# Kernel tuning notes

Hardware: AMD Instinct MI355X
Metric: run time of the kernel (lower is better)

## Reference

```python
import jax, jax.numpy as jnp
import numpy as np

D = 256      # d_model
H = 8        # n_heads
L = 4        # n_levels
P = 4        # n_points
DFF = 1024   # d_ffn
DH = D // H  # head dim
SPATIAL = np.array([[100, 100], [50, 50], [25, 25], [13, 13]], dtype=np.int64)  # (H_l, W_l)
LV = int((SPATIAL[:, 0] * SPATIAL[:, 1]).sum())  # 13294 flattened memory tokens


def layer_norm(x, w, b, eps=1e-5):
    m = jnp.mean(x, -1, keepdims=True)
    v = jnp.mean((x - m) ** 2, -1, keepdims=True)
    return (x - m) * jax.lax.rsqrt(v + eps) * w + b


def setup_inputs() -> dict:
    key = jax.random.key(0)
    ks = jax.random.split(key, 16)
    nq, bs = 900, 8

    def w(k, shape, s=0.02):
        return jax.random.normal(k, shape, dtype=jnp.float32) * s

    return {
        "tgt": jax.random.normal(ks[0], (nq, bs, D), jnp.float32),
        "tgt_query_pos": jax.random.normal(ks[1], (nq, bs, D), jnp.float32),
        "tgt_reference_points": jax.random.uniform(ks[2], (nq, bs, L, 2), jnp.float32),
        "memory": jax.random.normal(ks[3], (LV, bs, D), jnp.float32),
        "sa_Wqkv": w(ks[4], (3 * D, D)), "sa_bqkv": jnp.zeros((3 * D,), jnp.float32),
        "sa_Wo": w(ks[5], (D, D)), "sa_bo": jnp.zeros((D,), jnp.float32),
        "ln1_w": jnp.ones((D,), jnp.float32), "ln1_b": jnp.zeros((D,), jnp.float32),
        "ln2_w": jnp.ones((D,), jnp.float32), "ln2_b": jnp.zeros((D,), jnp.float32),
        "ln3_w": jnp.ones((D,), jnp.float32), "ln3_b": jnp.zeros((D,), jnp.float32),
        "ca_Woff": w(ks[6], (H * L * P * 2, D)), "ca_boff": w(ks[7], (H * L * P * 2,), 0.5),
        "ca_Wattn": w(ks[8], (H * L * P, D)), "ca_battn": jnp.zeros((H * L * P,), jnp.float32),
        "ca_Wval": w(ks[9], (D, D)), "ca_bval": jnp.zeros((D,), jnp.float32),
        "ca_Wout": w(ks[10], (D, D)), "ca_bout": jnp.zeros((D,), jnp.float32),
        "ffn_W1": w(ks[11], (DFF, D)), "ffn_b1": jnp.zeros((DFF,), jnp.float32),
        "ffn_W2": w(ks[12], (D, DFF)), "ffn_b2": jnp.zeros((D,), jnp.float32),
        "memory_key_padding_mask": jnp.zeros((bs, LV), jnp.bool_),
        "memory_spatial_shapes": jnp.asarray(SPATIAL),
    }


def msdeform_attn(query, ref, value, mask, shapes_np,
                  Woff, boff, Wattn, battn, Wval, bval, Wout, bout):
    # query: [bs,nq,D], ref: [bs,nq,L,2], value: [bs,lv,D], mask: [bs,lv]
    bs, nq, _ = query.shape
    lv = value.shape[1]
    v = value @ Wval.T + bval
    v = jnp.where(mask[:, :, None], 0.0, v)
    v = v.reshape(bs, lv, H, DH).transpose(0, 2, 1, 3)  # [bs,H,lv,DH]
    off = (query @ Woff.T + boff).reshape(bs, nq, H, L, P, 2)
    aw = jax.nn.softmax((query @ Wattn.T + battn).reshape(bs, nq, H, L * P), -1)
    aw = aw.reshape(bs, nq, H, L, P)
    # offset normalizer is [W_l, H_l]
    norm = jnp.asarray(shapes_np[:, ::-1].copy(), jnp.float32)  # [L,2]
    loc = ref[:, :, None, :, None, :] + off / norm[None, None, None, :, None, :]
    out = jnp.zeros((bs, nq, H, DH), jnp.float32)
    start = 0
    for l in range(L):
        Hl, Wl = int(shapes_np[l, 0]), int(shapes_np[l, 1])
        vf = v[:, :, start:start + Hl * Wl]  # [bs,H,Hl*Wl,DH]
        start += Hl * Wl
        # grid_sample(align_corners=False) pixel coords
        x = loc[:, :, :, l, :, 0] * Wl - 0.5  # [bs,nq,H,P]
        y = loc[:, :, :, l, :, 1] * Hl - 0.5
        x0 = jnp.floor(x); y0 = jnp.floor(y)
        fx = x - x0; fy = y - y0
        x0i = x0.astype(jnp.int32); y0i = y0.astype(jnp.int32)

        def gather(yi, xi):
            valid = ((xi >= 0) & (xi < Wl) & (yi >= 0) & (yi < Hl)).astype(jnp.float32)
            idx = jnp.clip(yi, 0, Hl - 1) * Wl + jnp.clip(xi, 0, Wl - 1)
            idx_t = idx.transpose(0, 2, 1, 3).reshape(bs, H, nq * P, 1)
            g = jnp.take_along_axis(vf, idx_t, axis=2)  # [bs,H,nq*P,DH]
            return g * valid.transpose(0, 2, 1, 3).reshape(bs, H, nq * P, 1)

        def wgt(w):
            return w.transpose(0, 2, 1, 3).reshape(bs, H, nq * P, 1)

        samp = (gather(y0i, x0i) * wgt((1 - fx) * (1 - fy))
                + gather(y0i, x0i + 1) * wgt(fx * (1 - fy))
                + gather(y0i + 1, x0i) * wgt((1 - fx) * fy)
                + gather(y0i + 1, x0i + 1) * wgt(fx * fy))
        samp = samp.reshape(bs, H, nq, P, DH)
        out = out + jnp.einsum('bhqpd,bqhp->bqhd', samp, aw[:, :, :, l])
    return out.reshape(bs, nq, D) @ Wout.T + bout


def reference(tgt, tgt_query_pos, tgt_reference_points, memory,
              sa_Wqkv, sa_bqkv, sa_Wo, sa_bo,
              ln1_w, ln1_b, ln2_w, ln2_b, ln3_w, ln3_b,
              ca_Woff, ca_boff, ca_Wattn, ca_battn, ca_Wval, ca_bval, ca_Wout, ca_bout,
              ffn_W1, ffn_b1, ffn_W2, ffn_b2,
              memory_key_padding_mask, memory_spatial_shapes):
    shapes_np = np.asarray(memory_spatial_shapes)  # static per trace
    nq, bs, _ = tgt.shape
    # --- self attention (post-LN, residual) ---
    q = tgt + tgt_query_pos
    qp = (q @ sa_Wqkv[:D].T + sa_bqkv[:D]).reshape(nq, bs, H, DH)
    kp = (q @ sa_Wqkv[D:2 * D].T + sa_bqkv[D:2 * D]).reshape(nq, bs, H, DH)
    vp = (tgt @ sa_Wqkv[2 * D:].T + sa_bqkv[2 * D:]).reshape(nq, bs, H, DH)
    scores = jnp.einsum('qbhd,kbhd->bhqk', qp, kp) * (1.0 / float(np.sqrt(DH)))
    attn = jax.nn.softmax(scores, -1)
    o = jnp.einsum('bhqk,kbhd->qbhd', attn, vp).reshape(nq, bs, D) @ sa_Wo.T + sa_bo
    tgt = layer_norm(tgt + o, ln2_w, ln2_b)
    # --- multi-scale deformable cross attention ---
    query = (tgt + tgt_query_pos).transpose(1, 0, 2)      # [bs,nq,D]
    ref = tgt_reference_points.transpose(1, 0, 2, 3)      # [bs,nq,L,2]
    val = memory.transpose(1, 0, 2)                       # [bs,lv,D]
    ca = msdeform_attn(query, ref, val, memory_key_padding_mask, shapes_np,
                       ca_Woff, ca_boff, ca_Wattn, ca_battn,
                       ca_Wval, ca_bval, ca_Wout, ca_bout).transpose(1, 0, 2)
    tgt = layer_norm(tgt + ca, ln1_w, ln1_b)
    # --- FFN ---
    t2 = jax.nn.relu(tgt @ ffn_W1.T + ffn_b1) @ ffn_W2.T + ffn_b2
    return layer_norm(tgt + t2, ln3_w, ln3_b)
```

## Files before the change

### kernel.cpp

```cpp
#include <hip/hip_runtime.h>
#include <hip/hip_bf16.h>

#define NQ   900
#define BSZ  8
#define DM   256
#define NH   8
#define DHD  32
#define DFF_ 1024
#define LVTOT 13294
#define NTOK (NQ*BSZ)
#define MVAL (LVTOT*BSZ)

typedef __attribute__((ext_vector_type(8))) short bf16x8;
typedef __attribute__((ext_vector_type(4))) short bf16x4;
typedef __attribute__((ext_vector_type(4))) float f32x4;
typedef unsigned int u32;

__device__ __forceinline__ unsigned short f2bf(float x) {
  union { __hip_bfloat16 h; unsigned short u; } cv;
  cv.h = __float2bfloat16(x);
  return cv.u;
}
__device__ __forceinline__ float bf2f(unsigned short u) {
  union { __hip_bfloat16 h; unsigned short u; } cv;
  cv.u = u;
  return __bfloat162float(cv.h);
}

__device__ __forceinline__ void gl_lds16(const void* gsrc, void* ldst) {
  __builtin_amdgcn_global_load_lds(
      (const __attribute__((address_space(1))) u32*)gsrc,
      (__attribute__((address_space(3))) u32*)ldst, 16, 0, 0);
}

__global__ __launch_bounds__(256) void prep_kernel(
    const float* p0, const float* p1, const float* p2, const float* p3,
    const float* p4, const float* p5, const float* p6, const float* p7,
    unsigned short* wdst,
    const float* a, const float* b, unsigned short* qdst,
    const float* boff, const float* battn, float* bcat) {
  int bid = blockIdx.x, tid = threadIdx.x;
  if (bid < 496) {
    long i8 = ((long)bid * 256 + tid) * 8;
    const float* src; long off;
    if      (i8 < 196608) { src = p0; off = i8; }
    else if (i8 < 262144) { src = p1; off = i8 - 196608; }
    else if (i8 < 327680) { src = p2; off = i8 - 262144; }
    else if (i8 < 393216) { src = p3; off = i8 - 327680; }
    else if (i8 < 425984) { src = p4; off = i8 - 393216; }
    else if (i8 < 491520) { src = p5; off = i8 - 425984; }
    else if (i8 < 753664) { src = p6; off = i8 - 491520; }
    else                  { src = p7; off = i8 - 753664; }
    float4 x = *(const float4*)(src + off);
    float4 y = *(const float4*)(src + off + 4);
    bf16x8 v;
    v[0] = (short)f2bf(x.x); v[1] = (short)f2bf(x.y);
    v[2] = (short)f2bf(x.z); v[3] = (short)f2bf(x.w);
    v[4] = (short)f2bf(y.x); v[5] = (short)f2bf(y.y);
    v[6] = (short)f2bf(y.z); v[7] = (short)f2bf(y.w);
    *(bf16x8*)(wdst + i8) = v;
  } else if (bid < 496 + 900) {
    int i = (bid - 496) * 256 + tid;
    float4 a0 = ((const float4*)a)[i * 2], a1 = ((const float4*)a)[i * 2 + 1];
    float4 b0 = ((const float4*)b)[i * 2], b1 = ((const float4*)b)[i * 2 + 1];
    bf16x8 v;
    v[0] = (short)f2bf(a0.x + b0.x); v[1] = (short)f2bf(a0.y + b0.y);
    v[2] = (short)f2bf(a0.z + b0.z); v[3] = (short)f2bf(a0.w + b0.w);
    v[4] = (short)f2bf(a1.x + b1.x); v[5] = (short)f2bf(a1.y + b1.y);
    v[6] = (short)f2bf(a1.z + b1.z); v[7] = (short)f2bf(a1.w + b1.w);
    *(bf16x8*)(qdst + (long)i * 8) = v;
  } else {
    int i = (bid - 1396) * 256 + tid;
    if (i < 256) bcat[i] = boff[i];
    else if (i < 384) bcat[i] = battn[i - 256];
  }
}


struct B3 {
  const void* A[3];
  const unsigned short* W[3];
  const float* bias[3];
  void* C[3];
  int M[3], ldc[3], af32[3], blk0[3], nx[3];
};

__global__ __launch_bounds__(256, 4) void gemm_batch3_kernel(B3 ops) {
  constexpr int K = 256, NSTEP = 4;
  __shared__ alignas(16) unsigned char As[32768];
  __shared__ alignas(16) unsigned char Bs[16384];
  int bid = blockIdx.x;
  int oi = (bid >= ops.blk0[2]) ? 2 : (bid >= ops.blk0[1] ? 1 : 0);
  int rel = bid - ops.blk0[oi];
  int nx = ops.nx[oi];
  int bx = rel % nx, by = rel / nx;
  const void* Araw = ops.A[oi];
  const unsigned short* W = ops.W[oi];
  const float* bias = ops.bias[oi];
  void* C = ops.C[oi];
  int M = ops.M[oi], ldc = ops.ldc[oi], AF32 = ops.af32[oi];

  int tid = threadIdx.x;
  int l = tid & 63, w = tid >> 6;
  int lr = l & 15, lg = l >> 4;
  int wr = w >> 1, wc = w & 1;
  int n0 = bx * 128, m0 = by * 128;
  int phase = by & (NSTEP - 1);

  f32x4 acc[4][4];
#pragma unroll
  for (int m = 0; m < 4; m++)
#pragma unroll
    for (int n = 0; n < 4; n++) acc[m][n] = (f32x4){0.f, 0.f, 0.f, 0.f};

  for (int tt = 0; tt < NSTEP; tt++) {
    int t = tt + phase; if (t >= NSTEP) t -= NSTEP;
    int k0 = t * 64;
    __syncthreads();
#pragma unroll
    for (int i4 = 0; i4 < 4; i4++) {
      int i = i4 * 4 + w;
      int row = i * 8 + (l >> 3);
      int sc = (l & 7) ^ (row & 7);
      gl_lds16(W + (long)(n0 + row) * K + k0 + sc * 8, Bs + i * 1024 + l * 16);
    }
    if (AF32) {
      const float* Af = (const float*)Araw;
#pragma unroll
      for (int i4 = 0; i4 < 8; i4++) {
        int i = i4 * 4 + w;
        int row = i * 4 + (l >> 4);
        int g = m0 + row; if (g >= M) g = M - 1;
        int sc = (l & 15) ^ (row & 15);
        gl_lds16(Af + (long)g * K + k0 + sc * 4, As + i * 1024 + l * 16);
      }
    } else {
      const unsigned short* A = (const unsigned short*)Araw;
#pragma unroll
      for (int i4 = 0; i4 < 4; i4++) {
        int i = i4 * 4 + w;
        int row = i * 8 + (l >> 3);
        int g = m0 + row; if (g >= M) g = M - 1;
        int sc = (l & 7) ^ (row & 7);
        gl_lds16(A + (long)g * K + k0 + sc * 8, As + i * 1024 + l * 16);
      }
    }
    __syncthreads();
#pragma unroll
    for (int sk = 0; sk < 2; sk++) {
      bf16x8 af[4], bfr[4];
      if (AF32) {
#pragma unroll
        for (int m = 0; m < 4; m++) {
          int row = wr * 64 + m * 16 + lr;
          int ca = (sk * 8 + lg * 2) ^ (row & 15);
          int cb = (sk * 8 + lg * 2 + 1) ^ (row & 15);
          f32x4 fa = *(const f32x4*)(As + row * 256 + ca * 16);
          f32x4 fb = *(const f32x4*)(As + row * 256 + cb * 16);
          bf16x8 v;
          v[0] = (short)f2bf(fa[0]); v[1] = (short)f2bf(fa[1]);
          v[2] = (short)f2bf(fa[2]); v[3] = (short)f2bf(fa[3]);
          v[4] = (short)f2bf(fb[0]); v[5] = (short)f2bf(fb[1]);
          v[6] = (short)f2bf(fb[2]); v[7] = (short)f2bf(fb[3]);
          af[m] = v;
        }
      } else {
#pragma unroll
        for (int m = 0; m < 4; m++) {
          int row = wr * 64 + m * 16 + lr;
          int c = (sk * 4 + lg) ^ (row & 7);
          af[m] = *(const bf16x8*)(As + row * 128 + c * 16);
        }
      }
#pragma unroll
      for (int n = 0; n < 4; n++) {
        int row = wc * 64 + n * 16 + lr;
        int c = (sk * 4 + lg) ^ (row & 7);
        bfr[n] = *(const bf16x8*)(Bs + row * 128 + c * 16);
      }
#pragma unroll
      for (int m = 0; m < 4; m++)
#pragma unroll
        for (int n = 0; n < 4; n++)
          acc[m][n] = __builtin_amdgcn_mfma_f32_16x16x32_bf16(af[m], bfr[n], acc[m][n], 0, 0, 0);
    }
  }

  float bv[4];
#pragma unroll
  for (int ni = 0; ni < 4; ni++) bv[ni] = bias[n0 + wc * 64 + ni * 16 + lr];
#pragma unroll
  for (int mi = 0; mi < 4; mi++) {
#pragma unroll
    for (int r = 0; r < 4; r++) {
      int row = m0 + wr * 64 + mi * 16 + lg * 4 + r;
      if (row < M) {
#pragma unroll
        for (int ni = 0; ni < 4; ni++) {
          int col = n0 + wc * 64 + ni * 16 + lr;
          ((unsigned short*)C)[(long)row * ldc + col] = f2bf(acc[mi][ni][r] + bv[ni]);
        }
      }
    }
  }
}

template <int AF32, int OUT_BF16, int RELU, int NSTEP>
__global__ __launch_bounds__(256, 4) void gemm_s_kernel(
    const void* __restrict__ Araw, const unsigned short* __restrict__ W,
    const float* __restrict__ bias, void* __restrict__ C,
    int M, int ldc) {
  constexpr int K = NSTEP * 64;
  constexpr int ABYTES = AF32 ? 32768 : 16384;
  __shared__ alignas(16) unsigned char As[ABYTES];
  __shared__ alignas(16) unsigned char Bs[16384];
  int tid = threadIdx.x;
  int l = tid & 63, w = tid >> 6;
  int lr = l & 15, lg = l >> 4;
  int wr = w >> 1, wc = w & 1;
  int n0 = blockIdx.x * 128, m0 = blockIdx.y * 128;
  int phase = blockIdx.y & (NSTEP - 1);

  f32x4 acc[4][4];
#pragma unroll
  for (int m = 0; m < 4; m++)
#pragma unroll
    for (int n = 0; n < 4; n++) acc[m][n] = (f32x4){0.f, 0.f, 0.f, 0.f};

  for (int tt = 0; tt < NSTEP; tt++) {
    int t = tt + phase; if (t >= NSTEP) t -= NSTEP;
    int k0 = t * 64;
    __syncthreads();
#pragma unroll
    for (int i4 = 0; i4 < 4; i4++) {
      int i = i4 * 4 + w;
      int row = i * 8 + (l >> 3);
      int sc = (l & 7) ^ (row & 7);
      gl_lds16(W + (long)(n0 + row) * K + k0 + sc * 8, Bs + i * 1024 + l * 16);
    }
    if (AF32) {
      const float* Af = (const float*)Araw;
#pragma unroll
      for (int i4 = 0; i4 < 8; i4++) {
        int i = i4 * 4 + w;
        int row = i * 4 + (l >> 4);
        int g = m0 + row; if (g >= M) g = M - 1;
        int sc = (l & 15) ^ (row & 15);
        gl_lds16(Af + (long)g * K + k0 + sc * 4, As + i * 1024 + l * 16);
      }
    } else {
      const unsigned short* A = (const unsigned short*)Araw;
#pragma unroll
      for (int i4 = 0; i4 < 4; i4++) {
        int i = i4 * 4 + w;
        int row = i * 8 + (l >> 3);
        int g = m0 + row; if (g >= M) g = M - 1;
        int sc = (l & 7) ^ (row & 7);
        gl_lds16(A + (long)g * K + k0 + sc * 8, As + i * 1024 + l * 16);
      }
    }
    __syncthreads();
#pragma unroll
    for (int sk = 0; sk < 2; sk++) {
      bf16x8 af[4], bfr[4];
      if (AF32) {
#pragma unroll
        for (int m = 0; m < 4; m++) {
          int row = wr * 64 + m * 16 + lr;
          int ca = (sk * 8 + lg * 2) ^ (row & 15);
          int cb = (sk * 8 + lg * 2 + 1) ^ (row & 15);
          f32x4 fa = *(const f32x4*)(As + row * 256 + ca * 16);
          f32x4 fb = *(const f32x4*)(As + row * 256 + cb * 16);
          bf16x8 v;
          v[0] = (short)f2bf(fa[0]); v[1] = (short)f2bf(fa[1]);
          v[2] = (short)f2bf(fa[2]); v[3] = (short)f2bf(fa[3]);
          v[4] = (short)f2bf(fb[0]); v[5] = (short)f2bf(fb[1]);
          v[6] = (short)f2bf(fb[2]); v[7] = (short)f2bf(fb[3]);
          af[m] = v;
        }
      } else {
#pragma unroll
        for (int m = 0; m < 4; m++) {
          int row = wr * 64 + m * 16 + lr;
          int c = (sk * 4 + lg) ^ (row & 7);
          af[m] = *(const bf16x8*)(As + row * 128 + c * 16);
        }
      }
#pragma unroll
      for (int n = 0; n < 4; n++) {
        int row = wc * 64 + n * 16 + lr;
        int c = (sk * 4 + lg) ^ (row & 7);
        bfr[n] = *(const bf16x8*)(Bs + row * 128 + c * 16);
      }
#pragma unroll
      for (int m = 0; m < 4; m++)
#pragma unroll
        for (int n = 0; n < 4; n++)
          acc[m][n] = __builtin_amdgcn_mfma_f32_16x16x32_bf16(af[m], bfr[n], acc[m][n], 0, 0, 0);
    }
  }

  float bv[4];
#pragma unroll
  for (int ni = 0; ni < 4; ni++) bv[ni] = bias[n0 + wc * 64 + ni * 16 + lr];
#pragma unroll
  for (int mi = 0; mi < 4; mi++) {
#pragma unroll
    for (int r = 0; r < 4; r++) {
      int row = m0 + wr * 64 + mi * 16 + lg * 4 + r;
      if (row < M) {
#pragma unroll
        for (int ni = 0; ni < 4; ni++) {
          int col = n0 + wc * 64 + ni * 16 + lr;
          float v = acc[mi][ni][r] + bv[ni];
          if (RELU) v = fmaxf(v, 0.f);
          if (OUT_BF16) ((unsigned short*)C)[(long)row * ldc + col] = f2bf(v);
          else          ((float*)C)[(long)row * ldc + col] = v;
        }
      }
    }
  }
}

__global__ __launch_bounds__(256) void attn_mfma_kernel(const unsigned short* __restrict__ qkv,
                                                        unsigned short* __restrict__ out) {
  __shared__ unsigned short Vt[32][72];
  __shared__ unsigned short Ps[4][16][72];
  int tid = threadIdx.x;
  int l = tid & 63, w = tid >> 6;
  int lr = l & 15, lg = l >> 4;
  int q0 = blockIdx.x * 64;
  int h = blockIdx.y & 7, b = blockIdx.y >> 3;
  const float scale = 0.17677669529663687f;

  int qrow = q0 + w * 16 + lr;
  int qclamp = qrow < 899 ? qrow : 899;
  bf16x8 qf = *(const bf16x8*)(qkv + ((long)qclamp * 8 + b) * 768 + h * 32 + lg * 8);

  f32x4 o_acc[2];
  o_acc[0] = (f32x4){0.f, 0.f, 0.f, 0.f};
  o_acc[1] = (f32x4){0.f, 0.f, 0.f, 0.f};
  float m_run[4] = {-1e30f, -1e30f, -1e30f, -1e30f};
  float l_run[4] = {0.f, 0.f, 0.f, 0.f};

  for (int k0 = 0; k0 < NQ; k0 += 64) {
    __syncthreads();
    {
      int key = tid >> 2, dg = tid & 3;
      int kk = k0 + key; if (kk > 899) kk = 899;
      bf16x8 vv = *(const bf16x8*)(qkv + ((long)kk * 8 + b) * 768 + 512 + h * 32 + dg * 8);
#pragma unroll
      for (int j = 0; j < 8; j++) Vt[dg * 8 + j][key] = (unsigned short)vv[j];
    }
    f32x4 sg[4];
#pragma unroll
    for (int ng = 0; ng < 4; ng++) {
      int key = k0 + ng * 16 + lr; int kc = key < 899 ? key : 899;
      bf16x8 kf = *(const bf16x8*)(qkv + ((long)kc * 8 + b) * 768 + 256 + h * 32 + lg * 8);
      sg[ng] = __builtin_amdgcn_mfma_f32_16x16x32_bf16(qf, kf, (f32x4){0.f, 0.f, 0.f, 0.f}, 0, 0, 0);
    }
    float sv[4][4];
#pragma unroll
    for (int ng = 0; ng < 4; ng++) {
      bool bad = (k0 + ng * 16 + lr) >= NQ;
#pragma unroll
      for (int r = 0; r < 4; r++) sv[ng][r] = bad ? -1e30f : sg[ng][r] * scale;
    }
    float p[4][4];
#pragma unroll
    for (int r = 0; r < 4; r++) {
      float rmax = fmaxf(fmaxf(sv[0][r], sv[1][r]), fmaxf(sv[2][r], sv[3][r]));
#pragma unroll
      for (int mk = 8; mk; mk >>= 1) rmax = fmaxf(rmax, __shfl_xor(rmax, mk));
      float mnew = fmaxf(m_run[r], rmax);
      float fs = __expf(m_run[r] - mnew);
      m_run[r] = mnew;
      float ps = 0.f;
#pragma unroll
      for (int ng = 0; ng < 4; ng++) { p[ng][r] = __expf(sv[ng][r] - mnew); ps += p[ng][r]; }
#pragma unroll
      for (int mk = 8; mk; mk >>= 1) ps += __shfl_xor(ps, mk);
      l_run[r] = l_run[r] * fs + ps;
      o_acc[0][r] *= fs;
      o_acc[1][r] *= fs;
    }
#pragma unroll
    for (int ng = 0; ng < 4; ng++)
#pragma unroll
      for (int r = 0; r < 4; r++)
        Ps[w][lg * 4 + r][lr + ng * 16] = f2bf(p[ng][r]);
    __syncthreads();
#pragma unroll
    for (int ks = 0; ks < 2; ks++) {
      bf16x8 pf = *(const bf16x8*)&Ps[w][lr][ks * 32 + lg * 8];
#pragma unroll
      for (int ni = 0; ni < 2; ni++) {
        bf16x8 vf = *(const bf16x8*)&Vt[ni * 16 + lr][ks * 32 + lg * 8];
        o_acc[ni] = __builtin_amdgcn_mfma_f32_16x16x32_bf16(pf, vf, o_acc[ni], 0, 0, 0);
      }
    }
  }
#pragma unroll
  for (int r = 0; r < 4; r++) {
    int orow = q0 + w * 16 + lg * 4 + r;
    if (orow < NQ) {
      float inv = 1.f / l_run[r];
      unsigned short* op = out + ((long)orow * 8 + b) * 256 + h * 32 + lr;
      op[0]  = f2bf(o_acc[0][r] * inv);
      op[16] = f2bf(o_acc[1][r] * inv);
    }
  }
}

__device__ __forceinline__ void fetch8_acc(const unsigned short* __restrict__ vtmp, int lo, int W,
                                           int yi, int xi, int b, int col0, float wgt,
                                           float* a) {
  if ((xi < 0) | (xi >= W) | (yi < 0) | (yi >= W)) return;
  const unsigned short* p = vtmp + ((long)((lo + yi * W + xi) * BSZ + b)) * 256 + col0;
  bf16x8 r = *(const bf16x8*)p;
#pragma unroll
  for (int j = 0; j < 8; j++) a[j] += wgt * bf2f((unsigned short)r[j]);
}

__global__ __launch_bounds__(256) void sampler_kernel(const unsigned short* __restrict__ vtmp,
                                                      const float* __restrict__ oa,
                                                      const float* __restrict__ ref,
                                                      unsigned short* __restrict__ samp) {
  __shared__ float s_off[8][256];
  __shared__ float s_aw[8][128];
  __shared__ float s_ref[8][8];
  int tid = threadIdx.x;
  int t0 = blockIdx.x * 8;
#pragma unroll
  for (int k = 0; k < 8; k++) s_off[k][tid] = oa[(long)(t0 + k) * 384 + tid];
#pragma unroll
  for (int i = 0; i < 4; i++) {
    int idx = i * 256 + tid;
    int k = idx >> 7, c = idx & 127;
    s_aw[k][c] = oa[(long)(t0 + k) * 384 + 256 + c];
  }
  if (tid < 64) s_ref[tid >> 3][tid & 7] = ref[(long)(t0 + (tid >> 3)) * 8 + (tid & 7)];
  __syncthreads();
  if (tid < 64) {
    int k = tid >> 3, hh = tid & 7;
    float* p = &s_aw[k][hh * 16];
    float m = -1e30f;
#pragma unroll
    for (int j = 0; j < 16; j++) m = fmaxf(m, p[j]);
    float s = 0.f;
#pragma unroll
    for (int j = 0; j < 16; j++) { p[j] = __expf(p[j] - m); s += p[j]; }
    float inv = 1.f / s;
#pragma unroll
    for (int j = 0; j < 16; j++) p[j] *= inv;
  }
  __syncthreads();
  int w = tid >> 5;
  int l = tid & 31;
  int t = t0 + w;
  int h = l >> 2, col0 = h * 32 + (l & 3) * 8;
  int b = t & 7;
  const int Wls[4]  = {100, 50, 25, 13};
  const int lofs[4] = {0, 10000, 12500, 13125};
  float a[8];
#pragma unroll
  for (int j = 0; j < 8; j++) a[j] = 0.f;
#pragma unroll
  for (int lvl = 0; lvl < 4; lvl++) {
    int W = Wls[lvl];
    float Wf = (float)W;
    int lo = lofs[lvl];
    float rx = s_ref[w][lvl * 2 + 0], ry = s_ref[w][lvl * 2 + 1];
#pragma unroll
    for (int p = 0; p < 4; p++) {
      float ox = s_off[w][((h * 4 + lvl) * 4 + p) * 2 + 0];
      float oy = s_off[w][((h * 4 + lvl) * 4 + p) * 2 + 1];
      float x = rx * Wf + ox - 0.5f;
      float y = ry * Wf + oy - 0.5f;
      float x0f = floorf(x), y0f = floorf(y);
      float fx = x - x0f, fy = y - y0f;
      int x0 = (int)x0f, y0 = (int)y0f;
      float aa = s_aw[w][h * 16 + lvl * 4 + p];
      float w00 = aa * (1.f - fx) * (1.f - fy);
      float w01 = aa * fx * (1.f - fy);
      float w10 = aa * (1.f - fx) * fy;
      float w11 = aa * fx * fy;
      fetch8_acc(vtmp, lo, W, y0,     x0,     b, col0, w00, a);
      fetch8_acc(vtmp, lo, W, y0,     x0 + 1, b, col0, w01, a);
      fetch8_acc(vtmp, lo, W, y0 + 1, x0,     b, col0, w10, a);
      fetch8_acc(vtmp, lo, W, y0 + 1, x0 + 1, b, col0, w11, a);
    }
  }
  bf16x8 o;
#pragma unroll
  for (int j = 0; j < 8; j++) o[j] = (short)f2bf(a[j]);
  *(bf16x8*)(samp + (long)t * 256 + col0) = o;
}

__global__ __launch_bounds__(256) void ln_kernel(const float* __restrict__ x,
                                                 const float* __restrict__ res,
                                                 const float* __restrict__ w,
                                                 const float* __restrict__ bvec,
                                                 float* __restrict__ out,
                                                 unsigned short* __restrict__ out_bf,
                                                 const float* __restrict__ pos,
                                                 unsigned short* __restrict__ pos_bf,
                                                 int rows) {
  int wv = threadIdx.x >> 6, lane = threadIdx.x & 63;
  int row = blockIdx.x * 4 + wv;
  if (row >= rows) return;
  float4 xv = *(const float4*)(x + (long)row * 256 + lane * 4);
  float4 rv = *(const float4*)(res + (long)row * 256 + lane * 4);
  float v0 = xv.x + rv.x, v1 = xv.y + rv.y, v2 = xv.z + rv.z, v3 = xv.w + rv.w;
  float s = v0 + v1 + v2 + v3;
#pragma unroll
  for (int o = 32; o; o >>= 1) s += __shfl_xor(s, o);
  float mean = s * (1.f / 256.f);
  float d0 = v0 - mean, d1 = v1 - mean, d2 = v2 - mean, d3 = v3 - mean;
  float q = d0 * d0 + d1 * d1 + d2 * d2 + d3 * d3;
#pragma unroll
  for (int o = 32; o; o >>= 1) q += __shfl_xor(q, o);
  float rstd = rsqrtf(q * (1.f / 256.f) + 1e-5f);
  float4 wv4 = *(const float4*)(w + lane * 4);
  float4 bv4 = *(const float4*)(bvec + lane * 4);
  float o0 = d0 * rstd * wv4.x + bv4.x;
  float o1 = d1 * rstd * wv4.y + bv4.y;
  float o2 = d2 * rstd * wv4.z + bv4.z;
  float o3 = d3 * rstd * wv4.w + bv4.w;
  *(float4*)(out + (long)row * 256 + lane * 4) = make_float4(o0, o1, o2, o3);
  if (out_bf) {
    unsigned short* p = out_bf + (long)row * 256 + lane * 4;
    p[0] = f2bf(o0); p[1] = f2bf(o1); p[2] = f2bf(o2); p[3] = f2bf(o3);
  }
  if (pos_bf) {
    float4 pv = *(const float4*)(pos + (long)row * 256 + lane * 4);
    unsigned short* p = pos_bf + (long)row * 256 + lane * 4;
    p[0] = f2bf(o0 + pv.x); p[1] = f2bf(o1 + pv.y);
    p[2] = f2bf(o2 + pv.z); p[3] = f2bf(o3 + pv.w);
  }
}

extern "C" void kernel_launch(void* const* d_in, const int* in_sizes, int n_in,
                              void* d_out, int out_size, void* d_ws, size_t ws_size,
                              hipStream_t stream) {
  const float* tgt     = (const float*)d_in[0];
  const float* pos     = (const float*)d_in[1];
  const float* refpts  = (const float*)d_in[2];
  const float* memory  = (const float*)d_in[3];
  const float* sa_Wqkv = (const float*)d_in[4];
  const float* sa_bqkv = (const float*)d_in[5];
  const float* sa_Wo   = (const float*)d_in[6];
  const float* sa_bo   = (const float*)d_in[7];
  const float* ln1_w   = (const float*)d_in[8];
  const float* ln1_b   = (const float*)d_in[9];
  const float* ln2_w   = (const float*)d_in[10];
  const float* ln2_b   = (const float*)d_in[11];
  const float* ln3_w   = (const float*)d_in[12];
  const float* ln3_b   = (const float*)d_in[13];
  const float* ca_Woff = (const float*)d_in[14];
  const float* ca_boff = (const float*)d_in[15];
  const float* ca_Wattn= (const float*)d_in[16];
  const float* ca_battn= (const float*)d_in[17];
  const float* ca_Wval = (const float*)d_in[18];
  const float* ca_bval = (const float*)d_in[19];
  const float* ca_Wout = (const float*)d_in[20];
  const float* ca_bout = (const float*)d_in[21];
  const float* ffn_W1  = (const float*)d_in[22];
  const float* ffn_b1  = (const float*)d_in[23];
  const float* ffn_W2  = (const float*)d_in[24];
  const float* ffn_b2  = (const float*)d_in[25];

  char* ws = (char*)d_ws;
  float*          buf_ca = (float*)(ws);
  float*          buf_t3 = (float*)(ws + 8388608);
  unsigned short* t3_bf  = (unsigned short*)(ws + 16777216);
  unsigned short* buf_h  = (unsigned short*)(ws + 20971520);
  float*          buf_f  = (float*)(ws + 36700160);
  float*          bias_cat = (float*)(ws + 44072960);
  unsigned short* buf_v  = (unsigned short*)(ws + 54452224);
  unsigned short* wts    = (unsigned short*)(ws + 112590848);
  unsigned short* buf_q  = (unsigned short*)(ws + 114622464);
  unsigned short* buf_qkv= (unsigned short*)(ws + 118308864);
  float*          buf_oa = (float*)(ws + 118308864);
  unsigned short* buf_o  = (unsigned short*)(ws + 129368064);
  unsigned short* buf_smp= (unsigned short*)(ws + 129368064);
  float*          buf_t2 = (float*)(ws + 133054464);

  const unsigned short* w_qkv = wts + 0;
  const unsigned short* w_o   = wts + 196608;
  const unsigned short* w_val = wts + 262144;
  const unsigned short* w_oa  = wts + 327680;
  const unsigned short* w_out = wts + 425984;
  const unsigned short* w_f1  = wts + 491520;
  const unsigned short* w_f2  = wts + 753664;

  dim3 blk(256);

  prep_kernel<<<1398, blk, 0, stream>>>(sa_Wqkv, sa_Wo, ca_Wval, ca_Woff, ca_Wattn,
                                        ca_Wout, ffn_W1, ffn_W2, wts,
                                        tgt, pos, buf_q, ca_boff, ca_battn, bias_cat);

  B3 ops;
  ops.A[0] = memory;   ops.W[0] = w_val;           ops.bias[0] = ca_bval;      ops.C[0] = buf_v;
  ops.M[0] = MVAL;     ops.ldc[0] = 256;           ops.af32[0] = 1;            ops.nx[0] = 2;
  ops.A[1] = buf_q;    ops.W[1] = w_qkv;           ops.bias[1] = sa_bqkv;      ops.C[1] = buf_qkv;
  ops.M[1] = NTOK;     ops.ldc[1] = 768;           ops.af32[1] = 0;            ops.nx[1] = 4;
  ops.A[2] = tgt;      ops.W[2] = w_qkv + 512*256; ops.bias[2] = sa_bqkv + 512; ops.C[2] = buf_qkv + 512;
  ops.M[2] = NTOK;     ops.ldc[2] = 768;           ops.af32[2] = 1;            ops.nx[2] = 2;
  ops.blk0[0] = 0; ops.blk0[1] = 1662; ops.blk0[2] = 1890;
  gemm_batch3_kernel<<<2004, blk, 0, stream>>>(ops);

  attn_mfma_kernel<<<dim3(15, 64), blk, 0, stream>>>(buf_qkv, buf_o);
  gemm_s_kernel<0, 0, 0, 4><<<dim3(2, 57), blk, 0, stream>>>(buf_o, w_o, sa_bo,
                                                             buf_t2, NTOK, 256);
  ln_kernel<<<1800, blk, 0, stream>>>(buf_t2, tgt, ln2_w, ln2_b, buf_t2, nullptr,
                                      pos, buf_q, NTOK);
  gemm_s_kernel<0, 0, 0, 4><<<dim3(3, 57), blk, 0, stream>>>(buf_q, w_oa, bias_cat,
                                                             buf_oa, NTOK, 384);
  sampler_kernel<<<NTOK / 8, blk, 0, stream>>>(buf_v, buf_oa, refpts, buf_smp);
  gemm_s_kernel<0, 0, 0, 4><<<dim3(2, 57), blk, 0, stream>>>(buf_smp, w_out, ca_bout,
                                                             buf_ca, NTOK, 256);
  ln_kernel<<<1800, blk, 0, stream>>>(buf_ca, buf_t2, ln1_w, ln1_b, buf_t3, t3_bf,
                                      nullptr, nullptr, NTOK);
  gemm_s_kernel<0, 1, 1, 4><<<dim3(8, 57), blk, 0, stream>>>(t3_bf, w_f1, ffn_b1,
                                                             buf_h, NTOK, 1024);
  gemm_s_kernel<0, 0, 0, 16><<<dim3(2, 57), blk, 0, stream>>>(buf_h, w_f2, ffn_b2,
                                                              buf_f, NTOK, 256);
  ln_kernel<<<1800, blk, 0, stream>>>(buf_f, buf_t3, ln3_w, ln3_b, (float*)d_out, nullptr,
                                      nullptr, nullptr, NTOK);
}
```

Before: 217.8 us.

## Fuse output-projection GEMMs with residual add and LayerNorm

Adds a gemm_ln kernel in which each block computes a full 64x256 row tile, adds bias and residual, reduces row mean and variance across warps through shared memory, and writes the normalized output plus an optional bf16 copy (with or without the positional embedding added). This replaces three GEMM+ln_kernel pairs, removing the separate LayerNorm launches and the fp32 intermediate round trips through memory. The cost is a grid of only 113 blocks and a one-pass variance formula that is less numerically robust.

```diff
diff --git a/kernel.cpp b/kernel.cpp
--- a/kernel.cpp
+++ b/kernel.cpp
@@ -76,7 +76,6 @@
   }
 }
 
-
 struct B3 {
   const void* A[3];
   const unsigned short* W[3];
@@ -320,6 +319,126 @@
       }
     }
   }
+}
+
+template <int NSTEP, int OUT2>
+__global__ __launch_bounds__(256, 4) void gemm_ln_kernel(
+    const unsigned short* __restrict__ A, const unsigned short* __restrict__ W,
+    const float* __restrict__ bias, const float* __restrict__ res,
+    const float* __restrict__ lnw, const float* __restrict__ lnb,
+    float* __restrict__ out, unsigned short* __restrict__ out2,
+    const float* __restrict__ pos, int M) {
+  constexpr int K = NSTEP * 64;
+  __shared__ alignas(16) unsigned char As[8192];
+  __shared__ alignas(16) unsigned char Bs[32768];
+  __shared__ float psum[4][64], psq[4][64];
+  int tid = threadIdx.x;
+  int l = tid & 63, w = tid >> 6;
+  int lr = l & 15, lg = l >> 4;
+  int m0 = blockIdx.x * 64;
+  int phase = blockIdx.x & (NSTEP - 1);
+
+  f32x4 acc[4][4];
+#pragma unroll
+  for (int m = 0; m < 4; m++)
+#pragma unroll
+    for (int n = 0; n < 4; n++) acc[m][n] = (f32x4){0.f, 0.f, 0.f, 0.f};
+
+  for (int tt = 0; tt < NSTEP; tt++) {
+    int t = tt + phase; if (t >= NSTEP) t -= NSTEP;
+    int k0 = t * 64;
+    __syncthreads();
+#pragma unroll
+    for (int j = 0; j < 2; j++) {
+      int lin = j * 256 + tid;
+      int row = lin >> 3, s = lin & 7;
+      int g = m0 + row; if (g >= M) g = M - 1;
+      int sc = s ^ (row & 7);
+      gl_lds16(A + (long)g * K + k0 + sc * 8, As + lin * 16);
+    }
+#pragma unroll
+    for (int j = 0; j < 8; j++) {
+      int lin = j * 256 + tid;
+      int row = lin >> 3, s = lin & 7;
+      int sc = s ^ (row & 7);
+      gl_lds16(W + (long)row * K + k0 + sc * 8, Bs + lin * 16);
+    }
+    __syncthreads();
+#pragma unroll
+    for (int sk = 0; sk < 2; sk++) {
+      bf16x8 af[4], bfr[4];
+#pragma unroll
+      for (int m = 0; m < 4; m++) {
+        int row = m * 16 + lr;
+        int c = (sk * 4 + lg) ^ (row & 7);
+        af[m] = *(const bf16x8*)(As + row * 128 + c * 16);
+      }
+#pragma unroll
+      for (int n = 0; n < 4; n++) {
+        int row = w * 64 + n * 16 + lr;
+        int c = (sk * 4 + lg) ^ (row & 7);
+        bfr[n] = *(const bf16x8*)(Bs + row * 128 + c * 16);
+      }
+#pragma unroll
+      for (int m = 0; m < 4; m++)
+#pragma unroll
+        for (int n = 0; n < 4; n++)
+          acc[m][n] = __builtin_amdgcn_mfma_f32_16x16x32_bf16(af[m], bfr[n], acc[m][n], 0, 0, 0);
+    }
+  }
+
+  float bv[4], lw[4], lb[4];
+#pragma unroll
+  for (int ni = 0; ni < 4; ni++) {
+    int col = w * 64 + ni * 16 + lr;
+    bv[ni] = bias[col]; lw[ni] = lnw[col]; lb[ni] = lnb[col];
+  }
+#pragma unroll
+  for (int mi = 0; mi < 4; mi++)
+#pragma unroll
+    for (int r2 = 0; r2 < 4; r2++) {
+      int row = m0 + mi * 16 + lg * 4 + r2;
+      int rc = row < M ? row : M - 1;
+#pragma unroll
+      for (int ni = 0; ni < 4; ni++)
+        acc[mi][ni][r2] += bv[ni] + res[(long)rc * 256 + w * 64 + ni * 16 + lr];
+    }
+#pragma unroll
+  for (int mi = 0; mi < 4; mi++)
+#pragma unroll
+    for (int r2 = 0; r2 < 4; r2++) {
+      float s = acc[mi][0][r2] + acc[mi][1][r2] + acc[mi][2][r2] + acc[mi][3][r2];
+      float q = acc[mi][0][r2] * acc[mi][0][r2] + acc[mi][1][r2] * acc[mi][1][r2] +
+                acc[mi][2][r2] * acc[mi][2][r2] + acc[mi][3][r2] * acc[mi][3][r2];
+#pragma unroll
+      for (int o = 1; o < 16; o <<= 1) { s += __shfl_xor(s, o); q += __shfl_xor(q, o); }
+      if (lr == 0) {
+        int lrow = mi * 16 + lg * 4 + r2;
+        psum[w][lrow] = s; psq[w][lrow] = q;
+      }
+    }
+  __syncthreads();
+#pragma unroll
+  for (int mi = 0; mi < 4; mi++)
+#pragma unroll
+    for (int r2 = 0; r2 < 4; r2++) {
+      int lrow = mi * 16 + lg * 4 + r2;
+      int row = m0 + lrow;
+      if (row >= M) continue;
+      float tot = psum[0][lrow] + psum[1][lrow] + psum[2][lrow] + psum[3][lrow];
+      float tq  = psq[0][lrow] + psq[1][lrow] + psq[2][lrow] + psq[3][lrow];
+      float mean = tot * (1.f / 256.f);
+      float var = tq * (1.f / 256.f) - mean * mean;
+      float rstd = rsqrtf(var + 1e-5f);
+#pragma unroll
+      for (int ni = 0; ni < 4; ni++) {
+        int col = w * 64 + ni * 16 + lr;
+        float o = (acc[mi][ni][r2] - mean) * rstd * lw[ni] + lb[ni];
+        out[(long)row * 256 + col] = o;
+        if (OUT2 == 1) out2[(long)row * 256 + col] = f2bf(o);
+        if (OUT2 == 2) out2[(long)row * 256 + col] = f2bf(o + pos[(long)row * 256 + col]);
+      }
+    }
 }
 
 __global__ __launch_bounds__(256) void attn_mfma_kernel(const unsigned short* __restrict__ qkv,
@@ -495,49 +614,6 @@
 #pragma unroll
   for (int j = 0; j < 8; j++) o[j] = (short)f2bf(a[j]);
   *(bf16x8*)(samp + (long)t * 256 + col0) = o;
-}
-
-__global__ __launch_bounds__(256) void ln_kernel(const float* __restrict__ x,
-                                                 const float* __restrict__ res,
-                                                 const float* __restrict__ w,
-                                                 const float* __restrict__ bvec,
-                                                 float* __restrict__ out,
-                                                 unsigned short* __restrict__ out_bf,
-                                                 const float* __restrict__ pos,
-                                                 unsigned short* __restrict__ pos_bf,
-                                                 int rows) {
-  int wv = threadIdx.x >> 6, lane = threadIdx.x & 63;
-  int row = blockIdx.x * 4 + wv;
-  if (row >= rows) return;
-  float4 xv = *(const float4*)(x + (long)row * 256 + lane * 4);
-  float4 rv = *(const float4*)(res + (long)row * 256 + lane * 4);
-  float v0 = xv.x + rv.x, v1 = xv.y + rv.y, v2 = xv.z + rv.z, v3 = xv.w + rv.w;
-  float s = v0 + v1 + v2 + v3;
-#pragma unroll
-  for (int o = 32; o; o >>= 1) s += __shfl_xor(s, o);
-  float mean = s * (1.f / 256.f);
-  float d0 = v0 - mean, d1 = v1 - mean, d2 = v2 - mean, d3 = v3 - mean;
-  float q = d0 * d0 + d1 * d1 + d2 * d2 + d3 * d3;
-#pragma unroll
-  for (int o = 32; o; o >>= 1) q += __shfl_xor(q, o);
-  float rstd = rsqrtf(q * (1.f / 256.f) + 1e-5f);
-  float4 wv4 = *(const float4*)(w + lane * 4);
-  float4 bv4 = *(const float4*)(bvec + lane * 4);
-  float o0 = d0 * rstd * wv4.x + bv4.x;
-  float o1 = d1 * rstd * wv4.y + bv4.y;
-  float o2 = d2 * rstd * wv4.z + bv4.z;
-  float o3 = d3 * rstd * wv4.w + bv4.w;
-  *(float4*)(out + (long)row * 256 + lane * 4) = make_float4(o0, o1, o2, o3);
-  if (out_bf) {
-    unsigned short* p = out_bf + (long)row * 256 + lane * 4;
-    p[0] = f2bf(o0); p[1] = f2bf(o1); p[2] = f2bf(o2); p[3] = f2bf(o3);
-  }
-  if (pos_bf) {
-    float4 pv = *(const float4*)(pos + (long)row * 256 + lane * 4);
-    unsigned short* p = pos_bf + (long)row * 256 + lane * 4;
-    p[0] = f2bf(o0 + pv.x); p[1] = f2bf(o1 + pv.y);
-    p[2] = f2bf(o2 + pv.z); p[3] = f2bf(o3 + pv.w);
-  }
 }
 
 extern "C" void kernel_launch(void* const* d_in, const int* in_sizes, int n_in,
@@ -575,7 +651,6 @@
   float*          buf_t3 = (float*)(ws + 8388608);
   unsigned short* t3_bf  = (unsigned short*)(ws + 16777216);
   unsigned short* buf_h  = (unsigned short*)(ws + 20971520);
-  float*          buf_f  = (float*)(ws + 36700160);
   float*          bias_cat = (float*)(ws + 44072960);
   unsigned short* buf_v  = (unsigned short*)(ws + 54452224);
   unsigned short* wts    = (unsigned short*)(ws + 112590848);
@@ -611,21 +686,17 @@
   gemm_batch3_kernel<<<2004, blk, 0, stream>>>(ops);
 
   attn_mfma_kernel<<<dim3(15, 64), blk, 0, stream>>>(buf_qkv, buf_o);
-  gemm_s_kernel<0, 0, 0, 4><<<dim3(2, 57), blk, 0, stream>>>(buf_o, w_o, sa_bo,
-                                                             buf_t2, NTOK, 256);
-  ln_kernel<<<1800, blk, 0, stream>>>(buf_t2, tgt, ln2_w, ln2_b, buf_t2, nullptr,
-                                      pos, buf_q, NTOK);
+
+  gemm_ln_kernel<4, 2><<<113, blk, 0, stream>>>(buf_o, w_o, sa_bo, tgt, ln2_w, ln2_b,
+                                                buf_t2, buf_q, pos, NTOK);
   gemm_s_kernel<0, 0, 0, 4><<<dim3(3, 57), blk, 0, stream>>>(buf_q, w_oa, bias_cat,
                                                              buf_oa, NTOK, 384);
   sampler_kernel<<<NTOK / 8, blk, 0, stream>>>(buf_v, buf_oa, refpts, buf_smp);
-  gemm_s_kernel<0, 0, 0, 4><<<dim3(2, 57), blk, 0, stream>>>(buf_smp, w_out, ca_bout,
-                                                             buf_ca, NTOK, 256);
-  ln_kernel<<<1800, blk, 0, stream>>>(buf_ca, buf_t2, ln1_w, ln1_b, buf_t3, t3_bf,
-                                      nullptr, nullptr, NTOK);
+  gemm_ln_kernel<4, 1><<<113, blk, 0, stream>>>(buf_smp, w_out, ca_bout, buf_t2,
+                                                ln1_w, ln1_b, buf_t3, t3_bf, nullptr, NTOK);
   gemm_s_kernel<0, 1, 1, 4><<<dim3(8, 57), blk, 0, stream>>>(t3_bf, w_f1, ffn_b1,
                                                              buf_h, NTOK, 1024);
-  gemm_s_kernel<0, 0, 0, 16><<<dim3(2, 57), blk, 0, stream>>>(buf_h, w_f2, ffn_b2,
-                                                              buf_f, NTOK, 256);
-  ln_kernel<<<1800, blk, 0, stream>>>(buf_f, buf_t3, ln3_w, ln3_b, (float*)d_out, nullptr,
-                                      nullptr, nullptr, NTOK);
-}
+  gemm_ln_kernel<16, 0><<<113, blk, 0, stream>>>(buf_h, w_f2, ffn_b2, buf_t3,
+                                                 ln3_w, ln3_b, (float*)d_out, nullptr,
+                                                 nullptr, NTOK);
+}
```

Measured after the change: 225.2 us. 1.03x slower.
